# Kernel optimization log

Hardware: AMD Instinct MI355X
Metric: run time of the kernel (lower is better)

The kernel has to match this reference:

```python
import jax, jax.numpy as jnp
import numpy as np

# Qwen3-Next-like dims
B, S, HID = 2, 2048, 2048
H, KV, D, ROT = 16, 2, 128, 32
G = H // KV              # kv repeat groups
SCALE = D ** -0.5
EPS = 1e-6
BETA_BIAS, BIAS_CAP = 1.0, 3.0   # L1 logit bias
BETA_POST = 0.5                  # L2 post-softmax rescale
ALPHA_K, ALPHA_V = 0.1, 0.1      # L4 k/v rescale
GMIN, GMAX = 0.9, 1.1
EMIN, EMAX = 0.9, 1.1


def setup_inputs() -> dict:
    key = jax.random.key(0)
    ks = jax.random.split(key, 10)
    hidden_states = jax.random.normal(ks[0], (B, S, HID), jnp.float32)
    # partial rotary embeddings (rot_dim = head_dim // 4)
    pos = jnp.arange(S, dtype=jnp.float32)
    inv = 1.0 / (10000.0 ** (jnp.arange(0, ROT, 2, dtype=jnp.float32) / ROT))
    freqs = pos[:, None] * inv[None, :]
    emb = jnp.concatenate([freqs, freqs], axis=-1)          # [S, ROT]
    cos = jnp.broadcast_to(jnp.cos(emb)[None], (B, S, ROT)).astype(jnp.float32)
    sin = jnp.broadcast_to(jnp.sin(emb)[None], (B, S, ROT)).astype(jnp.float32)
    # additive causal mask [B,1,S,S]
    causal = jnp.tril(jnp.ones((S, S), jnp.bool_))
    attention_mask = jnp.where(causal, 0.0, -1e9).astype(jnp.float32)
    attention_mask = jnp.broadcast_to(attention_mask[None, None], (B, 1, S, S))
    # key prior: positive, sums to 1 over kv_len
    prior = jax.nn.softmax(jax.random.normal(ks[1], (S,), jnp.float32))
    s = 0.02
    Wq = jax.random.normal(ks[2], (HID, H * D * 2), jnp.float32) * s
    Wk = jax.random.normal(ks[3], (HID, KV * D), jnp.float32) * s
    Wv = jax.random.normal(ks[4], (HID, KV * D), jnp.float32) * s
    Wo = jax.random.normal(ks[5], (H * D, HID), jnp.float32) * s
    q_norm_w = 1.0 + 0.02 * jax.random.normal(ks[6], (D,), jnp.float32)
    k_norm_w = 1.0 + 0.02 * jax.random.normal(ks[7], (D,), jnp.float32)
    return {"hidden_states": hidden_states, "cos": cos, "sin": sin,
            "attention_mask": attention_mask, "prior": prior,
            "Wq": Wq, "Wk": Wk, "Wv": Wv, "Wo": Wo,
            "q_norm_w": q_norm_w, "k_norm_w": k_norm_w}


def _rms(x, w):
    return x * jax.lax.rsqrt(jnp.mean(x * x, axis=-1, keepdims=True) + EPS) * w


def _rot_half(x):
    x1, x2 = jnp.split(x, 2, axis=-1)
    return jnp.concatenate([-x2, x1], axis=-1)


def _rope(x, cos, sin):
    # x: [B,h,S,D]; rotary on first ROT dims only (Qwen3-Next partial rotary)
    xr, xp = x[..., :ROT], x[..., ROT:]
    xr = xr * cos + _rot_half(xr) * sin
    return jnp.concatenate([xr, xp], axis=-1)


def reference(hidden_states, cos, sin, attention_mask, prior, Wq, Wk, Wv, Wo, q_norm_w, k_norm_w):
    h = hidden_states
    # gated q projection: chunk into query + gate
    qg = (h @ Wq).reshape(B, S, H, 2 * D)
    q, gate = qg[..., :D], qg[..., D:]
    gate = gate.reshape(B, S, H * D)
    q = _rms(q, q_norm_w).transpose(0, 2, 1, 3)                       # [B,H,S,D]
    k = _rms((h @ Wk).reshape(B, S, KV, D), k_norm_w).transpose(0, 2, 1, 3)  # [B,KV,S,D]
    v = (h @ Wv).reshape(B, S, KV, D).transpose(0, 2, 1, 3)
    c, s_ = cos[:, None], sin[:, None]                                # [B,1,S,ROT]
    q, k = _rope(q, c, s_), _rope(k, c, s_)
    k = jnp.repeat(k, G, axis=1)                                      # GQA expand -> [B,H,S,D]
    v = jnp.repeat(v, G, axis=1)
    # L4: prior-based elementwise k/v rescale with clamped gamma/eta
    pc = prior * S                                                    # mean ~1 over keys
    gamma = jnp.clip(1.0 + ALPHA_K * (pc - 1.0), GMIN, GMAX)
    eta = jnp.clip(1.0 + ALPHA_V * (pc - 1.0), EMIN, EMAX)
    k = k * gamma[None, None, :, None]
    v = v * eta[None, None, :, None]
    scores = jnp.einsum('bhqd,bhkd->bhqk', q, k) * SCALE
    # L1: capped steering bias on logits
    scores = scores + jnp.clip(BETA_BIAS * prior, -BIAS_CAP, BIAS_CAP)[None, None, None, :]
    scores = scores + attention_mask
    probs = jax.nn.softmax(scores.astype(jnp.float32), axis=-1)       # fp32 softmax
    # L2: post-softmax prior rescale + renorm
    p2 = probs * (1.0 + BETA_POST * pc)[None, None, None, :]
    probs = p2 / jnp.sum(p2, axis=-1, keepdims=True)
    out = jnp.einsum('bhqk,bhkd->bhqd', probs.astype(h.dtype), v)
    out = out.transpose(0, 2, 1, 3).reshape(B, S, H * D)
    out = out * jax.nn.sigmoid(gate)                                  # gated attention output
    return out @ Wo
```

## Files before the change

### kernel.cpp

```cpp
#include <hip/hip_runtime.h>
#include <hip/hip_bf16.h>
#include <stdint.h>

#define B_    2
#define S_    2048
#define HID_  2048
#define H_    16
#define KV_   2
#define D_    128
#define ROT_  32
#define QGS   4608
#define SCALE_ 0.08838834764831845f
#define LOG2E_ 1.44269504f

typedef __attribute__((ext_vector_type(8))) short  short8;
typedef __attribute__((ext_vector_type(4))) float  floatx4;

__device__ __forceinline__ float b2f(unsigned short u) {
  union { unsigned int i; float f; } v; v.i = ((unsigned int)u) << 16; return v.f;
}
__device__ __forceinline__ unsigned short f2b(float f) {
  union { float f; unsigned int i; } v; v.f = f;
  return (unsigned short)((v.i + 0x7fffu + ((v.i >> 16) & 1u)) >> 16);
}
__device__ __forceinline__ void gload_lds16(const unsigned short* g, unsigned short* l) {
  __builtin_amdgcn_global_load_lds((const __attribute__((address_space(1))) void*)g,
                                   (__attribute__((address_space(3))) void*)l, 16, 0, 0);
}

__device__ __forceinline__ void transpose_body(const float* __restrict__ in,
                                               unsigned short* __restrict__ out,
                                               int R, int C, int bx, int by, int t) {
  __shared__ unsigned short tile[64][68];
  int tx = t & 15, ty = t >> 4;
  long c0 = (long)bx * 64, r0 = (long)by * 64;
#pragma unroll
  for (int i = 0; i < 4; i++) {
    int row = ty + 16 * i;
    const float* src = in + (r0 + row) * C + c0 + 4 * tx;
    float4 v = *(const float4*)src;
    tile[row][4 * tx + 0] = f2b(v.x);
    tile[row][4 * tx + 1] = f2b(v.y);
    tile[row][4 * tx + 2] = f2b(v.z);
    tile[row][4 * tx + 3] = f2b(v.w);
  }
  __syncthreads();
#pragma unroll
  for (int i = 0; i < 4; i++) {
    int oc = ty + 16 * i;
    ushort4 v;
    v.x = tile[4 * tx + 0][oc];
    v.y = tile[4 * tx + 1][oc];
    v.z = tile[4 * tx + 2][oc];
    v.w = tile[4 * tx + 3][oc];
    *(ushort4*)(out + (c0 + oc) * R + r0 + 4 * tx) = v;
  }
}

__global__ __launch_bounds__(256) void k_preproc(const float* __restrict__ h_f,
                                                 const float* __restrict__ prior,
                                                 const float* __restrict__ Wq,
                                                 const float* __restrict__ Wk,
                                                 const float* __restrict__ Wv,
                                                 const float* __restrict__ Wo,
                                                 unsigned short* __restrict__ hbF,
                                                 unsigned short* __restrict__ WqkvT,
                                                 unsigned short* __restrict__ WoT,
                                                 float* __restrict__ ge,
                                                 float* __restrict__ kbias) {
  int bx = blockIdx.x;
  const int t = threadIdx.x;
  if (bx < 8) {
    int i = bx * 256 + t;
    float p  = prior[i];
    float pc = p * (float)S_;
    float g  = 1.0f + 0.1f * (pc - 1.0f);
    g = fminf(fmaxf(g, 0.9f), 1.1f);
    ge[i] = g;
    float cb = fminf(fmaxf(p, -3.0f), 3.0f);
    kbias[i] = (cb + logf(1.0f + 0.5f * pc)) * LOG2E_;
    return;
  }
  bx -= 8;
  if (bx < 4096) {
    long i0 = ((long)bx * 256 + t) * 8;
    float4 a = *(const float4*)(h_f + i0);
    float4 b = *(const float4*)(h_f + i0 + 4);
    short8 v;
    v[0] = (short)f2b(a.x); v[1] = (short)f2b(a.y);
    v[2] = (short)f2b(a.z); v[3] = (short)f2b(a.w);
    v[4] = (short)f2b(b.x); v[5] = (short)f2b(b.y);
    v[6] = (short)f2b(b.z); v[7] = (short)f2b(b.w);
    int row = (int)(i0 >> 11);
    int k   = (int)(i0 & 2047);
    size_t dst = ((size_t)((row >> 4) * 64 + (k >> 5))) * 512
               + (size_t)((row & 15) + ((k >> 3) & 3) * 16) * 8;
    *(short8*)(hbF + dst) = v;
    return;
  }
  bx -= 4096;
  if (bx < 2048) { transpose_body(Wq, WqkvT, 2048, 4096, bx & 63, bx >> 6, t); return; }
  bx -= 2048;
  if (bx < 1024) { transpose_body(Wo, WoT, 2048, 2048, bx & 31, bx >> 5, t); return; }
  bx -= 1024;
  if (bx < 128)  { transpose_body(Wk, WqkvT + (size_t)4096 * 2048, 2048, 256, bx & 3, bx >> 2, t); return; }
  bx -= 128;
  transpose_body(Wv, WqkvT + (size_t)4352 * 2048, 2048, 256, bx & 3, bx >> 2, t);
}

template <int OUT32>
__global__ __launch_bounds__(256, 4) void k_gemm_af(const unsigned short* __restrict__ aF,
                                                    const unsigned short* __restrict__ Bt,
                                                    void* __restrict__ Cv,
                                                    int M, int N, int K) {
  __shared__ __align__(16) unsigned short Bs[3][128 * 32];
  const int t    = threadIdx.x;
  const int lane = t & 63;
  const int wv   = t >> 6;
  const int wm   = wv >> 1, wn = wv & 1;
  const long m0  = (long)blockIdx.y * 128;
  const long n0  = (long)blockIdx.x * 128;
  const int r15  = lane & 15, g4 = lane >> 4;

  const int srow = lane >> 2;
  const int scol = ((lane & 3) ^ ((lane >> 3) & 3)) * 8;
  const unsigned short* sB0 = Bt + (n0 + wv * 16 + srow)       * K + scol;
  const unsigned short* sB1 = Bt + (n0 + (wv + 4) * 16 + srow) * K + scol;

  const int KC = K >> 5;
  const unsigned short* aBase = aF + ((size_t)(((m0 >> 4) + wm * 4) * KC)) * 512 + lane * 8;

  floatx4 acc[4][4];
#pragma unroll
  for (int m = 0; m < 4; m++)
#pragma unroll
    for (int n = 0; n < 4; n++) acc[m][n] = (floatx4){0.f, 0.f, 0.f, 0.f};

  const int nk = K >> 5;
  gload_lds16(sB0,      &Bs[0][wv * 512]);
  gload_lds16(sB1,      &Bs[0][(wv + 4) * 512]);
  gload_lds16(sB0 + 32, &Bs[1][wv * 512]);
  gload_lds16(sB1 + 32, &Bs[1][(wv + 4) * 512]);
  short8 afA[4], afB[4];
#pragma unroll
  for (int m = 0; m < 4; m++) afA[m] = *(const short8*)(aBase + (size_t)(m * KC) * 512);
#pragma unroll
  for (int m = 0; m < 4; m++) afB[m] = *(const short8*)(aBase + (size_t)(m * KC + 1) * 512);

  const int fcol = (g4 ^ ((r15 >> 1) & 3)) * 8;
  int cb = 0;
  for (int k2 = 0; k2 < nk; k2 += 2) {
    {
      const int k = k2;
      asm volatile("s_waitcnt vmcnt(10)" ::: "memory");
      __builtin_amdgcn_sched_barrier(0);
      __builtin_amdgcn_s_barrier();
      __builtin_amdgcn_sched_barrier(0);
      if (k + 2 < nk) {
        const int nb = (cb + 2 >= 3) ? cb - 1 : cb + 2;
        gload_lds16(sB0 + (k + 2) * 32, &Bs[nb][wv * 512]);
        gload_lds16(sB1 + (k + 2) * 32, &Bs[nb][(wv + 4) * 512]);
      }
      short8 bf[4];
#pragma unroll
      for (int n = 0; n < 4; n++)
        bf[n] = *(const short8*)(&Bs[cb][(wn * 64 + n * 16 + r15) * 32 + fcol]);
#pragma unroll
      for (int m = 0; m < 4; m++)
#pragma unroll
        for (int n = 0; n < 4; n++)
          acc[m][n] = __builtin_amdgcn_mfma_f32_16x16x32_bf16(afA[m], bf[n], acc[m][n], 0, 0, 0);
      if (k + 2 < nk) {
#pragma unroll
        for (int m = 0; m < 4; m++)
          afA[m] = *(const short8*)(aBase + (size_t)(m * KC + k + 2) * 512);
      }
      cb = (cb == 2) ? 0 : cb + 1;
    }
    {
      const int k = k2 + 1;
      if (k2 + 2 >= nk) asm volatile("s_waitcnt vmcnt(4)" ::: "memory");
      else              asm volatile("s_waitcnt vmcnt(10)" ::: "memory");
      __builtin_amdgcn_sched_barrier(0);
      __builtin_amdgcn_s_barrier();
      __builtin_amdgcn_sched_barrier(0);
      if (k + 2 < nk) {
        const int nb = (cb + 2 >= 3) ? cb - 1 : cb + 2;
        gload_lds16(sB0 + (k + 2) * 32, &Bs[nb][wv * 512]);
        gload_lds16(sB1 + (k + 2) * 32, &Bs[nb][(wv + 4) * 512]);
      }
      short8 bf[4];
#pragma unroll
      for (int n = 0; n < 4; n++)
        bf[n] = *(const short8*)(&Bs[cb][(wn * 64 + n * 16 + r15) * 32 + fcol]);
#pragma unroll
      for (int m = 0; m < 4; m++)
#pragma unroll
        for (int n = 0; n < 4; n++)
          acc[m][n] = __builtin_amdgcn_mfma_f32_16x16x32_bf16(afB[m], bf[n], acc[m][n], 0, 0, 0);
      if (k + 2 < nk) {
#pragma unroll
        for (int m = 0; m < 4; m++)
          afB[m] = *(const short8*)(aBase + (size_t)(m * KC + k + 2) * 512);
      }
      cb = (cb == 2) ? 0 : cb + 1;
    }
  }

#pragma unroll
  for (int m = 0; m < 4; m++) {
    const long rbase = m0 + wm * 64 + m * 16 + g4 * 4;
#pragma unroll
    for (int n = 0; n < 4; n++) {
      const long cidx = n0 + wn * 64 + n * 16 + r15;
#pragma unroll
      for (int i = 0; i < 4; i++) {
        if (OUT32) ((float*)Cv)[(rbase + i) * N + cidx] = acc[m][n][i];
        else ((unsigned short*)Cv)[(rbase + i) * N + cidx] = f2b(acc[m][n][i]);
      }
    }
  }
}

__global__ __launch_bounds__(256) void k_qkvpost(const unsigned short* __restrict__ qgkv,
                                                 const float* __restrict__ cosb,
                                                 const float* __restrict__ sinb,
                                                 const float* __restrict__ ge,
                                                 const float* __restrict__ knw,
                                                 unsigned short* __restrict__ kF,
                                                 unsigned short* __restrict__ vF) {
  int bxx = blockIdx.x;
  if (bxx < 2048) {
    int wid  = bxx * 4 + ((int)threadIdx.x >> 6);
    int lane = threadIdx.x & 63;
    int kvb  = wid & 1;
    long bs  = wid >> 1;
    int b = (int)(bs >> 11), s = (int)(bs & 2047);
    int d0 = lane * 2;

    const unsigned short* src = qgkv + bs * QGS + 4096 + kvb * 128 + d0;
    float x0 = b2f(src[0]), x1 = b2f(src[1]);
    float ss = x0 * x0 + x1 * x1;
#pragma unroll
    for (int mask = 1; mask < 64; mask <<= 1) ss += __shfl_xor(ss, mask);
    float rstd = rsqrtf(ss * (1.0f / 128.0f) + 1e-6f);
    float w0 = knw[d0], w1 = knw[d0 + 1];
    float xn0 = x0 * rstd * w0, xn1 = x1 * rstd * w1;
    float p0 = __shfl_xor(xn0, 8), p1 = __shfl_xor(xn1, 8);
    float y0 = xn0, y1 = xn1;
    if (lane < 16) {
      float c0 = cosb[bs * ROT_ + d0], c1 = cosb[bs * ROT_ + d0 + 1];
      float s0 = sinb[bs * ROT_ + d0], s1 = sinb[bs * ROT_ + d0 + 1];
      float sgn = (lane < 8) ? -1.0f : 1.0f;
      y0 = xn0 * c0 + sgn * p0 * s0;
      y1 = xn1 * c1 + sgn * p1 * s1;
    }
    float g = ge[s];
    unsigned int pack = (unsigned int)f2b(y0 * g) | ((unsigned int)f2b(y1 * g) << 16);
    size_t off = (size_t)(b * KV_ + kvb) * 262144
               + (size_t)((s >> 4) * 4 + (d0 >> 5)) * 512
               + (size_t)(((s & 15) + (((d0 >> 3) & 3)) * 16)) * 8 + (d0 & 7);
    *(unsigned int*)(kF + off) = pack;
  } else {
    int bx  = bxx - 2048;
    int scn = bx & 7, d = (bx >> 3) & 127, kvb = (bx >> 10) & 1, b = bx >> 11;
    int s = scn * 256 + threadIdx.x;
    float v = b2f(qgkv[((long)(b * S_ + s)) * QGS + 4352 + kvb * 128 + d]);
    v *= ge[s];
    size_t off = (size_t)(b * KV_ + kvb) * 262144
               + (size_t)((s >> 6) * 16 + (d >> 4) * 2 + ((s >> 5) & 1)) * 512
               + (size_t)((d & 15) + ((s >> 3) & 3) * 16) * 8 + (s & 7);
    vF[off] = f2b(v);
  }
}

__global__ __launch_bounds__(256) void k_attn(const unsigned short* __restrict__ qgkv,
                                              const unsigned short* __restrict__ kF,
                                              const unsigned short* __restrict__ vF,
                                              const float* __restrict__ kbias,
                                              const float* __restrict__ cosb,
                                              const float* __restrict__ sinb,
                                              const float* __restrict__ qnw,
                                              unsigned short* __restrict__ agF) {
  __shared__ __align__(16) unsigned short KL[2][8192];
  __shared__ __align__(16) unsigned short Ps[4][16 * 88];
  const int t = threadIdx.x;
  const int lane = t & 63, wv = t >> 6;
  const int r15 = lane & 15, g4 = lane >> 4;
  const int p = blockIdx.x;
  const int xcd = p & 7;
  const int grp = xcd >> 1;
  const int mem = ((p >> 3) << 1) | (xcd & 1);
  const int head = mem & 7;
  const int quad = 31 - (mem >> 3);
  const int b = grp >> 1, kvh = grp & 1;
  const int hh = kvh * 8 + head;
  const int strip = quad * 4 + wv;
  const int q0s = strip * 16;
  const int ntiles = quad + 1;

  const unsigned short* kFg = kF + (size_t)(b * KV_ + kvh) * 262144;
  const unsigned short* vFg = vF + (size_t)(b * KV_ + kvh) * 262144;

  short8 qf[4];
  {
    const int q = q0s + r15;
    const unsigned short* qp = qgkv + ((size_t)(b * S_) + q) * QGS + hh * 256 + g4 * 8;
    float xn[4][8];
    float ssq = 0.f;
#pragma unroll
    for (int kb = 0; kb < 4; kb++) {
      short8 qr = *(const short8*)(qp + kb * 32);
#pragma unroll
      for (int e = 0; e < 8; e++) {
        float x = b2f((unsigned short)qr[e]);
        xn[kb][e] = x;
        ssq += x * x;
      }
    }
    ssq += __shfl_xor(ssq, 16);
    ssq += __shfl_xor(ssq, 32);
    float rstd = rsqrtf(ssq * (1.0f / 128.0f) + 1e-6f) * (SCALE_ * LOG2E_);
#pragma unroll
    for (int kb = 0; kb < 4; kb++) {
      float4 w0 = *(const float4*)(&qnw[kb * 32 + g4 * 8]);
      float4 w1 = *(const float4*)(&qnw[kb * 32 + g4 * 8 + 4]);
      xn[kb][0] *= rstd * w0.x; xn[kb][1] *= rstd * w0.y;
      xn[kb][2] *= rstd * w0.z; xn[kb][3] *= rstd * w0.w;
      xn[kb][4] *= rstd * w1.x; xn[kb][5] *= rstd * w1.y;
      xn[kb][6] *= rstd * w1.z; xn[kb][7] *= rstd * w1.w;
    }
    {
      const float* cbp = cosb + ((size_t)(b * S_) + q) * ROT_ + g4 * 8;
      const float* sbp = sinb + ((size_t)(b * S_) + q) * ROT_ + g4 * 8;
      float4 c0 = *(const float4*)(cbp), c1 = *(const float4*)(cbp + 4);
      float4 s0 = *(const float4*)(sbp), s1 = *(const float4*)(sbp + 4);
      float cv[8] = {c0.x, c0.y, c0.z, c0.w, c1.x, c1.y, c1.z, c1.w};
      float sv[8] = {s0.x, s0.y, s0.z, s0.w, s1.x, s1.y, s1.z, s1.w};
      float sgn = (g4 < 2) ? -1.0f : 1.0f;
#pragma unroll
      for (int e = 0; e < 8; e++) {
        float part = __shfl_xor(xn[0][e], 32);
        xn[0][e] = xn[0][e] * cv[e] + sgn * part * sv[e];
      }
    }
#pragma unroll
    for (int kb = 0; kb < 4; kb++)
#pragma unroll
      for (int e = 0; e < 8; e++) qf[kb][e] = (short)f2b(xn[kb][e]);
  }

  floatx4 oacc[8];
#pragma unroll
  for (int nd = 0; nd < 8; nd++) oacc[nd] = (floatx4){0.f, 0.f, 0.f, 0.f};
  float mrow = -1e30f, lrw = 0.f;

#pragma unroll
  for (int i = 0; i < 4; i++)
    gload_lds16(kFg + (size_t)wv * 2048 + i * 512 + lane * 8, &KL[0][wv * 2048 + i * 512]);
  __syncthreads();

  int cur = 0;
  for (int tile = 0; tile < ntiles; tile++) {
    if (tile + 1 < ntiles) {
      const size_t src = (size_t)(tile + 1) * 8192 + wv * 2048 + lane * 8;
#pragma unroll
      for (int i = 0; i < 4; i++)
        gload_lds16(kFg + src + i * 512, &KL[cur ^ 1][wv * 2048 + i * 512]);
    }

    floatx4 sacc[4];
#pragma unroll
    for (int n = 0; n < 4; n++) sacc[n] = (floatx4){0.f, 0.f, 0.f, 0.f};
    __builtin_amdgcn_s_setprio(1);
#pragma unroll
    for (int n = 0; n < 4; n++) {
      const unsigned short* kl = &KL[cur][n * 2048 + lane * 8];
      short8 a0 = *(const short8*)(kl);
      short8 a1 = *(const short8*)(kl + 512);
      short8 a2 = *(const short8*)(kl + 1024);
      short8 a3 = *(const short8*)(kl + 1536);
      sacc[n] = __builtin_amdgcn_mfma_f32_16x16x32_bf16(a0, qf[0], sacc[n], 0, 0, 0);
      sacc[n] = __builtin_amdgcn_mfma_f32_16x16x32_bf16(a1, qf[1], sacc[n], 0, 0, 0);
      sacc[n] = __builtin_amdgcn_mfma_f32_16x16x32_bf16(a2, qf[2], sacc[n], 0, 0, 0);
      sacc[n] = __builtin_amdgcn_mfma_f32_16x16x32_bf16(a3, qf[3], sacc[n], 0, 0, 0);
    }
    __builtin_amdgcn_s_setprio(0);

    const unsigned short* vt = vFg + (size_t)tile * 8192 + lane * 8;
    short8 vfA[8];
#pragma unroll
    for (int nd = 0; nd < 8; nd++) vfA[nd] = *(const short8*)(vt + (nd * 2) * 512);

    const bool last = (tile == ntiles - 1);
    float scf[4][4];
#pragma unroll
    for (int n = 0; n < 4; n++) {
      const int j0 = tile * 64;
      float4 kb4 = *(const float4*)(&kbias[j0 + n * 16 + g4 * 4]);
#pragma unroll
      for (int i = 0; i < 4; i++) {
        float kbv = (i == 0) ? kb4.x : (i == 1) ? kb4.y : (i == 2) ? kb4.z : kb4.w;
        float v = sacc[n][i] + kbv;
        if (last) {
          int jg = j0 + n * 16 + g4 * 4 + i;
          if (jg > q0s + r15) v = -1e30f;
        }
        scf[n][i] = v;
      }
    }
    float pmax = scf[0][0];
#pragma unroll
    for (int n = 0; n < 4; n++)
#pragma unroll
      for (int i = 0; i < 4; i++) pmax = fmaxf(pmax, scf[n][i]);
    pmax = fmaxf(pmax, __shfl_xor(pmax, 16));
    pmax = fmaxf(pmax, __shfl_xor(pmax, 32));
    if (__any(pmax > mrow + 11.5f)) {
      float mn = fmaxf(mrow, pmax);
      float aq = exp2f(mrow - mn);
      mrow = mn;
      lrw *= aq;
      float ai[4];
#pragma unroll
      for (int i = 0; i < 4; i++) ai[i] = __shfl(aq, g4 * 4 + i);
#pragma unroll
      for (int nd = 0; nd < 8; nd++)
#pragma unroll
        for (int i = 0; i < 4; i++) oacc[nd][i] *= ai[i];
    }
    float rsum = 0.f;
#pragma unroll
    for (int n = 0; n < 4; n++)
#pragma unroll
      for (int i = 0; i < 4; i++) {
        float pv = exp2f(scf[n][i] - mrow);
        scf[n][i] = pv;
        rsum += pv;
      }
    rsum += __shfl_xor(rsum, 16);
    rsum += __shfl_xor(rsum, 32);
    lrw += rsum;

#pragma unroll
    for (int n = 0; n < 4; n++) {
      unsigned int r0, r1;
      asm("v_cvt_pk_bf16_f32 %0, %1, %2" : "=v"(r0) : "v"(scf[n][0]), "v"(scf[n][1]));
      asm("v_cvt_pk_bf16_f32 %0, %1, %2" : "=v"(r1) : "v"(scf[n][2]), "v"(scf[n][3]));
      uint2 w; w.x = r0; w.y = r1;
      *(uint2*)(&Ps[wv][r15 * 88 + n * 16 + g4 * 4]) = w;
    }

    short8 vfB[8];
#pragma unroll
    for (int nd = 0; nd < 8; nd++) vfB[nd] = *(const short8*)(vt + (nd * 2 + 1) * 512);

    {
      __builtin_amdgcn_s_setprio(1);
      short8 pa0 = *(const short8*)(&Ps[wv][r15 * 88 + g4 * 8]);
#pragma unroll
      for (int nd = 0; nd < 8; nd++)
        oacc[nd] = __builtin_amdgcn_mfma_f32_16x16x32_bf16(pa0, vfA[nd], oacc[nd], 0, 0, 0);
      short8 pa1 = *(const short8*)(&Ps[wv][r15 * 88 + 32 + g4 * 8]);
#pragma unroll
      for (int nd = 0; nd < 8; nd++)
        oacc[nd] = __builtin_amdgcn_mfma_f32_16x16x32_bf16(pa1, vfB[nd], oacc[nd], 0, 0, 0);
      __builtin_amdgcn_s_setprio(0);
    }
    __syncthreads();
    cur ^= 1;
  }

  float il[4];
#pragma unroll
  for (int i = 0; i < 4; i++) il[i] = __shfl(lrw, g4 * 4 + i);
  unsigned short* aBase = agF + (size_t)(b * 128 + strip) * 64 * 512;
#pragma unroll
  for (int i = 0; i < 4; i++) {
    int q = q0s + g4 * 4 + i;
    float inv = 1.0f / il[i];
    const unsigned short* gptr = qgkv + ((size_t)(b * S_ + q)) * QGS + hh * 256 + 128;
#pragma unroll
    for (int nd = 0; nd < 8; nd++) {
      int d = nd * 16 + r15;
      float gt = b2f(gptr[d]);
      float sg = 1.0f / (1.0f + __expf(-gt));
      size_t idx = (size_t)(hh * 4 + (d >> 5)) * 512
                 + (size_t)((g4 * 4 + i) + ((d >> 3) & 3) * 16) * 8 + (d & 7);
      aBase[idx] = f2b(oacc[nd][i] * inv * sg);
    }
  }
}

extern "C" void kernel_launch(void* const* d_in, const int* in_sizes, int n_in,
                              void* d_out, int out_size, void* d_ws, size_t ws_size,
                              hipStream_t stream) {
  const float* h_f   = (const float*)d_in[0];
  const float* cosb  = (const float*)d_in[1];
  const float* sinb  = (const float*)d_in[2];
  const float* prior = (const float*)d_in[4];
  const float* Wq    = (const float*)d_in[5];
  const float* Wk    = (const float*)d_in[6];
  const float* Wv    = (const float*)d_in[7];
  const float* Wo    = (const float*)d_in[8];
  const float* qnw   = (const float*)d_in[9];
  const float* knw   = (const float*)d_in[10];

  char* ws = (char*)d_ws;
  size_t off = 0;
  auto alloc = [&](size_t bytes) { char* p = ws + off; off += (bytes + 255) & ~(size_t)255; return p; };
  unsigned short* hbF   = (unsigned short*)alloc((size_t)4096 * 2048 * 2);
  unsigned short* WqkvT = (unsigned short*)alloc((size_t)4608 * 2048 * 2);
  unsigned short* WoT   = (unsigned short*)alloc((size_t)2048 * 2048 * 2);
  unsigned short* qgkv  = (unsigned short*)alloc((size_t)4096 * QGS * 2);
  unsigned short* kF    = (unsigned short*)alloc((size_t)B_ * KV_ * S_ * D_ * 2);
  unsigned short* vF    = (unsigned short*)alloc((size_t)B_ * KV_ * S_ * D_ * 2);
  float* ge    = (float*)alloc((size_t)S_ * 4);
  float* kbias = (float*)alloc((size_t)S_ * 4);
  unsigned short* agF = hbF;

  dim3 blk(256);
  k_preproc<<<dim3(7432), blk, 0, stream>>>(h_f, prior, Wq, Wk, Wv, Wo,
                                            hbF, WqkvT, WoT, ge, kbias);
  k_gemm_af<0><<<dim3(36, 32), blk, 0, stream>>>(hbF, WqkvT, qgkv, 4096, QGS, 2048);
  k_qkvpost<<<dim3(6144), blk, 0, stream>>>(qgkv, cosb, sinb, ge, knw, kF, vF);
  k_attn<<<dim3(1024), blk, 0, stream>>>(qgkv, kF, vF, kbias, cosb, sinb, qnw, agF);
  k_gemm_af<1><<<dim3(16, 32), blk, 0, stream>>>(agF, WoT, d_out, 4096, 2048, 2048);
}
```

Before: 258.8 us.

## Restructure GEMM B-tile pipeline to 4-buffer double-step with one barrier per pair

The GEMM main loop moves from a 3-slot LDS ring with a barrier every k-step to 4 LDS slots used as two ping-pong pairs. Each iteration issues global-to-LDS loads for two future k-steps at once and syncs only once per two steps. This is meant to halve barrier count and lengthen the window for async loads to complete. In exchange it uses more LDS per block, which may reduce occupancy, and the waitcnt accounting changes.

Result: faster. 248.6 us (-4.0%).

```diff
diff --git a/kernel.cpp b/kernel.cpp
--- a/kernel.cpp
+++ b/kernel.cpp
@@ -113,7 +113,7 @@
                                                     const unsigned short* __restrict__ Bt,
                                                     void* __restrict__ Cv,
                                                     int M, int N, int K) {
-  __shared__ __align__(16) unsigned short Bs[3][128 * 32];
+  __shared__ __align__(16) unsigned short Bs[4][128 * 32];
   const int t    = threadIdx.x;
   const int lane = t & 63;
   const int wv   = t >> 6;
@@ -141,70 +141,62 @@
   gload_lds16(sB1,      &Bs[0][(wv + 4) * 512]);
   gload_lds16(sB0 + 32, &Bs[1][wv * 512]);
   gload_lds16(sB1 + 32, &Bs[1][(wv + 4) * 512]);
+  __builtin_amdgcn_sched_barrier(0);
   short8 afA[4], afB[4];
 #pragma unroll
   for (int m = 0; m < 4; m++) afA[m] = *(const short8*)(aBase + (size_t)(m * KC) * 512);
 #pragma unroll
   for (int m = 0; m < 4; m++) afB[m] = *(const short8*)(aBase + (size_t)(m * KC + 1) * 512);
+  __builtin_amdgcn_sched_barrier(0);
 
   const int fcol = (g4 ^ ((r15 >> 1) & 3)) * 8;
-  int cb = 0;
-  for (int k2 = 0; k2 < nk; k2 += 2) {
+  int rb = 0;
+  for (int k = 0; k < nk; k += 2) {
+    asm volatile("s_waitcnt vmcnt(8)" ::: "memory");
+    __builtin_amdgcn_sched_barrier(0);
+    __builtin_amdgcn_s_barrier();
+    __builtin_amdgcn_sched_barrier(0);
+    const bool more = (k + 2 < nk);
+    if (more) {
+      const int wb = rb ^ 2;
+      gload_lds16(sB0 + (k + 2) * 32, &Bs[wb][wv * 512]);
+      gload_lds16(sB1 + (k + 2) * 32, &Bs[wb][(wv + 4) * 512]);
+      gload_lds16(sB0 + (k + 3) * 32, &Bs[wb + 1][wv * 512]);
+      gload_lds16(sB1 + (k + 3) * 32, &Bs[wb + 1][(wv + 4) * 512]);
+    }
     {
-      const int k = k2;
-      asm volatile("s_waitcnt vmcnt(10)" ::: "memory");
-      __builtin_amdgcn_sched_barrier(0);
-      __builtin_amdgcn_s_barrier();
-      __builtin_amdgcn_sched_barrier(0);
-      if (k + 2 < nk) {
-        const int nb = (cb + 2 >= 3) ? cb - 1 : cb + 2;
-        gload_lds16(sB0 + (k + 2) * 32, &Bs[nb][wv * 512]);
-        gload_lds16(sB1 + (k + 2) * 32, &Bs[nb][(wv + 4) * 512]);
-      }
       short8 bf[4];
 #pragma unroll
       for (int n = 0; n < 4; n++)
-        bf[n] = *(const short8*)(&Bs[cb][(wn * 64 + n * 16 + r15) * 32 + fcol]);
+        bf[n] = *(const short8*)(&Bs[rb][(wn * 64 + n * 16 + r15) * 32 + fcol]);
 #pragma unroll
       for (int m = 0; m < 4; m++)
 #pragma unroll
         for (int n = 0; n < 4; n++)
           acc[m][n] = __builtin_amdgcn_mfma_f32_16x16x32_bf16(afA[m], bf[n], acc[m][n], 0, 0, 0);
-      if (k + 2 < nk) {
-#pragma unroll
-        for (int m = 0; m < 4; m++)
-          afA[m] = *(const short8*)(aBase + (size_t)(m * KC + k + 2) * 512);
-      }
-      cb = (cb == 2) ? 0 : cb + 1;
+    }
+    if (more) {
+#pragma unroll
+      for (int m = 0; m < 4; m++)
+        afA[m] = *(const short8*)(aBase + (size_t)(m * KC + k + 2) * 512);
     }
     {
-      const int k = k2 + 1;
-      if (k2 + 2 >= nk) asm volatile("s_waitcnt vmcnt(4)" ::: "memory");
-      else              asm volatile("s_waitcnt vmcnt(10)" ::: "memory");
-      __builtin_amdgcn_sched_barrier(0);
-      __builtin_amdgcn_s_barrier();
-      __builtin_amdgcn_sched_barrier(0);
-      if (k + 2 < nk) {
-        const int nb = (cb + 2 >= 3) ? cb - 1 : cb + 2;
-        gload_lds16(sB0 + (k + 2) * 32, &Bs[nb][wv * 512]);
-        gload_lds16(sB1 + (k + 2) * 32, &Bs[nb][(wv + 4) * 512]);
-      }
       short8 bf[4];
 #pragma unroll
       for (int n = 0; n < 4; n++)
-        bf[n] = *(const short8*)(&Bs[cb][(wn * 64 + n * 16 + r15) * 32 + fcol]);
+        bf[n] = *(const short8*)(&Bs[rb + 1][(wn * 64 + n * 16 + r15) * 32 + fcol]);
 #pragma unroll
       for (int m = 0; m < 4; m++)
 #pragma unroll
         for (int n = 0; n < 4; n++)
           acc[m][n] = __builtin_amdgcn_mfma_f32_16x16x32_bf16(afB[m], bf[n], acc[m][n], 0, 0, 0);
-      if (k + 2 < nk) {
-#pragma unroll
-        for (int m = 0; m < 4; m++)
-          afB[m] = *(const short8*)(aBase + (size_t)(m * KC + k + 2) * 512);
-      }
-      cb = (cb == 2) ? 0 : cb + 1;
-    }
+    }
+    if (more) {
+#pragma unroll
+      for (int m = 0; m < 4; m++)
+        afB[m] = *(const short8*)(aBase + (size_t)(m * KC + k + 3) * 512);
+    }
+    rb ^= 2;
   }
 
 #pragma unroll
```
